# Performance work log

Hardware: AMD Instinct MI355X
Metric: run time of the kernel (lower is better)

## Reference

```python
import jax, jax.numpy as jnp
import numpy as np
import math

B, L, D, H, NL, V, C = 32, 512, 512, 8, 4, 32000, 2
DK = D // H
DFF = 4 * D
EPS = 1e-5


def _pos_encoding(max_len, d):
    pos = np.arange(max_len)[:, None].astype(np.float32)
    div = np.exp(np.arange(0, d, 2).astype(np.float32) * (-math.log(10000.0) / d))
    pe = np.zeros((max_len, d), np.float32)
    pe[:, 0::2] = np.sin(pos * div)
    pe[:, 1::2] = np.cos(pos * div)
    return jnp.asarray(pe)


def setup_inputs() -> dict:
    key = jax.random.key(0)
    keys = iter(jax.random.split(key, 64))
    s = 0.02
    def nrm(shape):
        return jax.random.normal(next(keys), shape, jnp.float32) * s
    emb = nrm((V, D)).at[0].set(0.0)  # padding_idx=0 row zeroed
    return {
        "x": jax.random.randint(next(keys), (B, L), 0, V),
        "mask": jnp.zeros((B, L), bool),
        "emb": emb,
        "pe": _pos_encoding(L, D),
        "Wq": nrm((NL, D, D)), "bq": jnp.zeros((NL, D)),
        "Wk": nrm((NL, D, D)), "bk": jnp.zeros((NL, D)),
        "Wv": nrm((NL, D, D)), "bv": jnp.zeros((NL, D)),
        "Wo": nrm((NL, D, D)), "bo": jnp.zeros((NL, D)),
        "ln1_g": jnp.ones((NL, D)), "ln1_b": jnp.zeros((NL, D)),
        "ln2_g": jnp.ones((NL, D)), "ln2_b": jnp.zeros((NL, D)),
        "ffW1": nrm((NL, D, DFF)), "ffb1": jnp.zeros((NL, DFF)),
        "ffW2": nrm((NL, DFF, D)), "ffb2": jnp.zeros((NL, D)),
        "lnf_g": jnp.ones((D,)), "lnf_b": jnp.zeros((D,)),
        "cW1": nrm((D, D)), "cb1": jnp.zeros((D,)),
        "cW2": nrm((D, C)), "cb2": jnp.zeros((C,)),
    }


def _layernorm(x, g, b):
    mu = jnp.mean(x, axis=-1, keepdims=True)
    var = jnp.mean((x - mu) ** 2, axis=-1, keepdims=True)
    return (x - mu) / jnp.sqrt(var + EPS) * g + b


def reference(x, mask, emb, pe, Wq, bq, Wk, bk, Wv, bv, Wo, bo,
              ln1_g, ln1_b, ln2_g, ln2_b, ffW1, ffb1, ffW2, ffb2,
              lnf_g, lnf_b, cW1, cb1, cW2, cb2):
    Bx, Lx = x.shape
    h = emb[x] * math.sqrt(D) + pe[None, :Lx, :]  # [B,L,D]
    key_mask = mask[:, None, None, :]  # [B,1,1,L]
    for i in range(NL):
        # --- multi-head attention (pre-norm1) ---
        hn = _layernorm(h, ln1_g[i], ln1_b[i])
        q = (hn @ Wq[i] + bq[i]).reshape(Bx, Lx, H, DK)
        k = (hn @ Wk[i] + bk[i]).reshape(Bx, Lx, H, DK)
        v = (hn @ Wv[i] + bv[i]).reshape(Bx, Lx, H, DK)
        scores = jnp.einsum('bqhd,bkhd->bhqk', q, k) / math.sqrt(DK)
        scores = jnp.where(key_mask, -jnp.inf, scores)
        attn = jax.nn.softmax(scores, axis=-1)
        ctx = jnp.einsum('bhqk,bkhd->bqhd', attn, v).reshape(Bx, Lx, D)
        h = h + ctx @ Wo[i] + bo[i]
        # --- feed-forward (pre-norm2), exact (erf) GELU like torch default ---
        hn2 = _layernorm(h, ln2_g[i], ln2_b[i])
        ff = jax.nn.gelu(hn2 @ ffW1[i] + ffb1[i], approximate=False) @ ffW2[i] + ffb2[i]
        h = h + ff
    h = _layernorm(h, lnf_g, lnf_b)
    pooled = jnp.mean(h, axis=1)  # [B,D]
    logits = jax.nn.gelu(pooled @ cW1 + cb1, approximate=False) @ cW2 + cb2
    return logits
```

## Files before the change

kernel.cpp:

```cpp
#include <hip/hip_runtime.h>
#include <hip/hip_bf16.h>

typedef __bf16 bf16_t;
typedef __bf16 bf16x8 __attribute__((ext_vector_type(8)));
typedef float  f32x4  __attribute__((ext_vector_type(4)));

#define NTOK 16384
#define DMODEL 512
#define SEQL 512
#define NLAY 4

typedef const __attribute__((address_space(1))) void* gas_t;
typedef __attribute__((address_space(3))) void* las_t;
__device__ __forceinline__ void gl16(const void* g, void* s){
  __builtin_amdgcn_global_load_lds((gas_t)g, (las_t)s, 16, 0, 0);
}

__device__ __forceinline__ f32x4 mfma16(bf16x8 a, bf16x8 b, f32x4 c){
  return __builtin_amdgcn_mfma_f32_16x16x32_bf16(a, b, c, 0, 0, 0);
}
__device__ __forceinline__ float geluf(float x){
  return 0.5f * x * (1.0f + erff(x * 0.70710678118654752f));
}
__device__ __forceinline__ float loadf(const void* p, long i, bool f32){
  return f32 ? ((const float*)p)[i] : (float)((const bf16_t*)p)[i];
}

__global__ void sniff_kernel(const unsigned int* __restrict__ emb_u, int* __restrict__ flag){
  if (threadIdx.x == 0){
    unsigned int u = emb_u[300] | emb_u[350] | emb_u[400] | emb_u[450];
    *flag = (u == 0u) ? 1 : 0;
  }
}

__global__ void transpose_kernel(const void* __restrict__ in, bf16_t* __restrict__ out,
                                 int R, int C, const int* __restrict__ flag){
  const bool f32 = (*flag != 0);
  __shared__ bf16_t tile[32][33];
  const long zo = (long)blockIdx.z * R * C;
  const int c0 = blockIdx.x * 32, r0 = blockIdx.y * 32;
  const int tx = threadIdx.x, ty = threadIdx.y;
  for (int i = 0; i < 4; i++){
    long idx = zo + (long)(r0 + ty + i*8) * C + (c0 + tx);
    tile[ty + i*8][tx] = (bf16_t)loadf(in, idx, f32);
  }
  __syncthreads();
  for (int i = 0; i < 4; i++){
    out[zo + (long)(c0 + ty + i*8) * R + (r0 + tx)] = tile[tx][ty + i*8];
  }
}

__global__ void transpose_qkv_kernel(const void* __restrict__ Wq, const void* __restrict__ Wk,
                                     const void* __restrict__ Wv, bf16_t* __restrict__ out,
                                     const int* __restrict__ flag){
  const bool f32 = (*flag != 0);
  __shared__ bf16_t tile[32][33];
  const int z = blockIdx.z, lz = z / 3, s = z % 3;
  const void* in = (s == 0) ? Wq : (s == 1) ? Wk : Wv;
  const long zi = (long)lz * 262144;
  const int c0 = blockIdx.x * 32, r0 = blockIdx.y * 32;
  const int tx = threadIdx.x, ty = threadIdx.y;
  for (int i = 0; i < 4; i++){
    long idx = zi + (long)(r0 + ty + i*8) * 512 + (c0 + tx);
    tile[ty + i*8][tx] = (bf16_t)loadf(in, idx, f32);
  }
  __syncthreads();
  for (int i = 0; i < 4; i++){
    out[(long)lz * 786432 + (long)(s*512 + c0 + ty + i*8) * 512 + (r0 + tx)] = tile[tx][ty + i*8];
  }
}

__global__ void biasprep_kernel(const void* bq, const void* bk, const void* bv,
                                const void* bo, const void* fb1, const void* fb2,
                                float* bqkvF, float* boF, float* fb1F, float* fb2F,
                                const int* __restrict__ flag){
  const bool f32 = (*flag != 0);
  const int z = blockIdx.y;
  const int idx = blockIdx.x * 256 + threadIdx.x;
  if (idx < 1536){
    const void* src = (idx < 512) ? bq : (idx < 1024) ? bk : bv;
    bqkvF[z*1536 + idx] = loadf(src, (long)z*512 + (idx & 511), f32);
  } else if (idx < 2048){
    boF[z*512 + idx - 1536] = loadf(bo, (long)z*512 + idx - 1536, f32);
  } else if (idx < 4096){
    fb1F[z*2048 + idx - 2048] = loadf(fb1, (long)z*2048 + idx - 2048, f32);
  } else {
    fb2F[z*512 + idx - 4096] = loadf(fb2, (long)z*512 + idx - 4096, f32);
  }
}

__global__ void embed_kernel(const int* __restrict__ x, const void* __restrict__ emb,
                             const void* __restrict__ pe, float* __restrict__ h,
                             const int* __restrict__ flag){
  const bool f32 = (*flag != 0);
  const int n = blockIdx.x;
  const int tok = x[n];
  const int l = n & (SEQL - 1);
  for (int d = threadIdx.x; d < DMODEL; d += 256){
    h[(long)n*DMODEL + d] = loadf(emb, (long)tok*DMODEL + d, f32) * 22.62741699796952f
                          + loadf(pe, (long)l*DMODEL + d, f32);
  }
}

__global__ void ln_kernel(const float* __restrict__ in, const void* __restrict__ g,
                          const void* __restrict__ b, long gboff, bf16_t* __restrict__ out,
                          const int* __restrict__ flag){
  const bool f32 = (*flag != 0);
  const int row = blockIdx.x, t = threadIdx.x;
  const float* r = in + (long)row * DMODEL;
  float v0 = r[t], v1 = r[t + 256];
  __shared__ float sb[4];
  float s = v0 + v1;
  #pragma unroll
  for (int o = 32; o > 0; o >>= 1) s += __shfl_down(s, o);
  if ((t & 63) == 0) sb[t >> 6] = s;
  __syncthreads();
  float mu = (sb[0] + sb[1] + sb[2] + sb[3]) * (1.f / DMODEL);
  __syncthreads();
  float d0 = v0 - mu, d1 = v1 - mu;
  s = d0*d0 + d1*d1;
  #pragma unroll
  for (int o = 32; o > 0; o >>= 1) s += __shfl_down(s, o);
  if ((t & 63) == 0) sb[t >> 6] = s;
  __syncthreads();
  float var = (sb[0] + sb[1] + sb[2] + sb[3]) * (1.f / DMODEL);
  float rstd = rsqrtf(var + 1e-5f);
  out[(long)row*DMODEL + t]       = (bf16_t)(d0*rstd*loadf(g, gboff + t, f32)       + loadf(b, gboff + t, f32));
  out[(long)row*DMODEL + t + 256] = (bf16_t)(d1*rstd*loadf(g, gboff + t + 256, f32) + loadf(b, gboff + t + 256, f32));
}

template<int MODE>
__global__ __launch_bounds__(256) void gemm_kernel(
    const bf16_t* __restrict__ A, const bf16_t* __restrict__ Bt,
    const float* __restrict__ bias,
    bf16_t* __restrict__ outB, float* __restrict__ outF, int K){
  __shared__ __align__(16) bf16_t S[4][8192];
  const int t = threadIdx.x;
  const int n0 = blockIdx.y * 128, m0 = blockIdx.x * 128;
  const int M = gridDim.x * 128;
  const int l = t & 63, w = t >> 6;
  const int lm = l & 15, g = l >> 4;
  const int wr = (w >> 1) * 64, wc = (w & 1) * 64;
  const f32x4 z4 = {0.f, 0.f, 0.f, 0.f};
  f32x4 acc[4][4];
  #pragma unroll
  for (int i = 0; i < 4; i++)
    #pragma unroll
    for (int j = 0; j < 4; j++) acc[i][j] = z4;
  const int offA0 = w*2048 + l*16;
  const int offA1 = offA0 + 1024;
  const bf16_t* gA0 = A  + (long)(n0 + (offA0 >> 6))*K + ((offA0 & 63) >> 1);
  const bf16_t* gA1 = A  + (long)(n0 + (offA1 >> 6))*K + ((offA1 & 63) >> 1);
  const bf16_t* gB0 = Bt + (long)(m0 + (offA0 >> 6))*K + ((offA0 & 63) >> 1);
  const bf16_t* gB1 = Bt + (long)(m0 + (offA1 >> 6))*K + ((offA1 & 63) >> 1);
  const int NT = K >> 5;
  #pragma unroll
  for (int pt = 0; pt < 3; ++pt){
    bf16_t* sb = &S[pt][0];
    const int ko = pt * 32;
    gl16(gA0 + ko, sb + w*1024);
    gl16(gA1 + ko, sb + w*1024 + 512);
    gl16(gB0 + ko, sb + 4096 + w*1024);
    gl16(gB1 + ko, sb + 4096 + w*1024 + 512);
  }
  for (int tt = 0; tt < NT; ++tt){
    const int tc = (tt + 3 < NT) ? (tt + 3) : (NT - 1);
    bf16_t* sb = &S[(tt + 3) & 3][0];
    const int ko = tc * 32;
    gl16(gA0 + ko, sb + w*1024);
    gl16(gA1 + ko, sb + w*1024 + 512);
    gl16(gB0 + ko, sb + 4096 + w*1024);
    gl16(gB1 + ko, sb + 4096 + w*1024 + 512);
    asm volatile("s_waitcnt vmcnt(12)" ::: "memory");
    __builtin_amdgcn_s_barrier();
    __builtin_amdgcn_sched_barrier(0);
    const bf16_t* As = &S[tt & 3][0];
    const bf16_t* Bs = As + 4096;
    bf16x8 af[4], bfr[4];
    #pragma unroll
    for (int i = 0; i < 4; i++) af[i]  = *(const bf16x8*)&As[(wr + i*16 + lm)*32 + g*8];
    #pragma unroll
    for (int j = 0; j < 4; j++) bfr[j] = *(const bf16x8*)&Bs[(wc + j*16 + lm)*32 + g*8];
    __builtin_amdgcn_s_setprio(1);
    #pragma unroll
    for (int i = 0; i < 4; i++)
      #pragma unroll
      for (int j = 0; j < 4; j++)
        acc[i][j] = mfma16(af[i], bfr[j], acc[i][j]);
    __builtin_amdgcn_s_setprio(0);
    __builtin_amdgcn_s_barrier();
    __builtin_amdgcn_sched_barrier(0);
  }
  asm volatile("s_waitcnt vmcnt(0)" ::: "memory");
  __syncthreads();
  if (MODE == 1){
    #pragma unroll
    for (int j = 0; j < 4; j++){
      const int m = m0 + wc + j*16 + lm;
      const float bv = bias[m];
      #pragma unroll
      for (int i = 0; i < 4; i++){
        const int nb = n0 + wr + i*16 + g*4;
        #pragma unroll
        for (int r = 0; r < 4; r++) outF[(long)(nb + r)*M + m] += acc[i][j][r] + bv;
      }
    }
  } else {
    bf16_t* Cs = &S[0][0] + w*1152;
    #pragma unroll
    for (int i = 0; i < 4; i++){
      #pragma unroll
      for (int j = 0; j < 4; j++){
        const float bv = bias[m0 + wc + j*16 + lm];
        #pragma unroll
        for (int r = 0; r < 4; r++){
          float v = acc[i][j][r] + bv;
          if (MODE == 2) v = geluf(v);
          Cs[(g*4 + r)*72 + j*16 + lm] = (bf16_t)v;
        }
      }
      const int row16 = l >> 2, ch = l & 3;
      #pragma unroll
      for (int cc = 0; cc < 2; cc++){
        const int chunk = cc*4 + ch;
        bf16x8 vv = *(const bf16x8*)&Cs[row16*72 + chunk*8];
        *(bf16x8*)&outB[(long)(n0 + wr + i*16 + row16)*M + m0 + wc + chunk*8] = vv;
      }
    }
  }
}

__global__ __launch_bounds__(64) void attn_kernel(
    const bf16_t* __restrict__ QKV, bf16_t* __restrict__ Op){
  const int l = threadIdx.x;
  const int lm = l & 15, g = l >> 4;
  const int qc = blockIdx.x;
  const int hh = blockIdx.y;
  const int bb = blockIdx.z;
  const long base = (long)bb * SEQL;
  const int hc = hh * 64;
  const int QS = 1536;
  const int q0 = qc * 64;
  bf16x8 qf[4][2];
  #pragma unroll
  for (int i = 0; i < 4; i++){
    const bf16_t* qrow = QKV + (base + q0 + i*16 + lm)*QS + hc + g*8;
    qf[i][0] = *(const bf16x8*)(qrow);
    qf[i][1] = *(const bf16x8*)(qrow + 32);
  }
  const f32x4 z4 = {0.f, 0.f, 0.f, 0.f};
  f32x4 oa[4][4];
  #pragma unroll
  for (int i = 0; i < 4; i++)
    #pragma unroll
    for (int dt = 0; dt < 4; dt++) oa[i][dt] = z4;
  float m_run[4], l_run[4];
  #pragma unroll
  for (int i = 0; i < 4; i++){ m_run[i] = -1e30f; l_run[i] = 0.f; }

  for (int kt = 0; kt < SEQL/32; ++kt){
    const int kcb = kt * 32;
    const bf16_t* kr0 = QKV + (base + kcb + lm)*QS + 512 + hc + g*8;
    const bf16_t* kr1 = kr0 + 16*QS;
    bf16x8 kf00 = *(const bf16x8*)(kr0);
    bf16x8 kf01 = *(const bf16x8*)(kr0 + 32);
    bf16x8 kf10 = *(const bf16x8*)(kr1);
    bf16x8 kf11 = *(const bf16x8*)(kr1 + 32);
    bf16x8 pa[4];
    #pragma unroll
    for (int i = 0; i < 4; i++){
      f32x4 s0 = z4, s1 = z4;
      __builtin_amdgcn_s_setprio(1);
      s0 = mfma16(kf00, qf[i][0], s0);
      s0 = mfma16(kf01, qf[i][1], s0);
      s1 = mfma16(kf10, qf[i][0], s1);
      s1 = mfma16(kf11, qf[i][1], s1);
      __builtin_amdgcn_s_setprio(0);
      float p[8]; float tmax = -1e30f;
      #pragma unroll
      for (int r = 0; r < 4; r++){ p[r] = s0[r]*0.125f; p[4+r] = s1[r]*0.125f; }
      #pragma unroll
      for (int j2 = 0; j2 < 8; j2++) tmax = fmaxf(tmax, p[j2]);
      tmax = fmaxf(tmax, __shfl_xor(tmax, 16));
      tmax = fmaxf(tmax, __shfl_xor(tmax, 32));
      const float mn = fmaxf(m_run[i], tmax);
      float ts = 0.f;
      #pragma unroll
      for (int j2 = 0; j2 < 8; j2++){ p[j2] = __expf(p[j2] - mn); ts += p[j2]; }
      ts += __shfl_xor(ts, 16);
      ts += __shfl_xor(ts, 32);
      const float alpha = __expf(m_run[i] - mn);
      l_run[i] = l_run[i] * alpha + ts;
      m_run[i] = mn;
      f32x4 alv;
      #pragma unroll
      for (int r = 0; r < 4; r++) alv[r] = __shfl(alpha, g*4 + r);
      #pragma unroll
      for (int dt = 0; dt < 4; dt++) oa[i][dt] *= alv;
      #pragma unroll
      for (int j2 = 0; j2 < 8; j2++) pa[i][j2] = (bf16_t)p[j2];
    }
    bf16x8 vf[4];
    #pragma unroll
    for (int j2 = 0; j2 < 8; j2++){
      const int pk = (j2 < 4) ? (g*4 + j2) : (16 + g*4 + (j2 - 4));
      const bf16_t* vr = QKV + (base + kcb + pk)*QS + 1024 + hc + lm;
      #pragma unroll
      for (int dt = 0; dt < 4; dt++) vf[dt][j2] = vr[dt*16];
    }
    __builtin_amdgcn_s_setprio(1);
    #pragma unroll
    for (int i = 0; i < 4; i++)
      #pragma unroll
      for (int dt = 0; dt < 4; dt++) oa[i][dt] = mfma16(pa[i], vf[dt], oa[i][dt]);
    __builtin_amdgcn_s_setprio(0);
  }
  #pragma unroll
  for (int i = 0; i < 4; i++){
    const float invl = 1.f / l_run[i];
    f32x4 inv;
    #pragma unroll
    for (int r = 0; r < 4; r++) inv[r] = __shfl(invl, g*4 + r);
    #pragma unroll
    for (int dt = 0; dt < 4; dt++)
      #pragma unroll
      for (int r = 0; r < 4; r++)
        Op[(base + q0 + i*16 + g*4 + r)*DMODEL + hc + dt*16 + lm] = (bf16_t)(oa[i][dt][r] * inv[r]);
  }
}

__global__ void pool_kernel(const bf16_t* __restrict__ hn, float* __restrict__ pooled){
  const int b = blockIdx.x, d = threadIdx.x;
  float a = 0.f;
  for (int s = 0; s < SEQL; s++) a += (float)hn[((long)b*SEQL + s)*DMODEL + d];
  pooled[b*DMODEL + d] = a * (1.f / SEQL);
}

__global__ void cls1_kernel(const float* __restrict__ pooled, const void* __restrict__ w1,
                            const void* __restrict__ b1, float* __restrict__ t1,
                            const int* __restrict__ flag){
  const bool f32 = (*flag != 0);
  const int b = blockIdx.x, m = threadIdx.x;
  const float* p = pooled + b * DMODEL;
  float a = 0.f;
  for (int d = 0; d < DMODEL; d++) a += p[d] * loadf(w1, (long)d*DMODEL + m, f32);
  t1[b*DMODEL + m] = geluf(a + loadf(b1, m, f32));
}

__global__ void cls2_kernel(const float* __restrict__ t1, const void* __restrict__ w2,
                            const void* __restrict__ b2, void* __restrict__ outp,
                            const int* __restrict__ flag){
  const bool f32 = (*flag != 0);
  const int i = threadIdx.x;
  if (i >= 64) return;
  const int b = i >> 1, c = i & 1;
  float a = 0.f;
  for (int m = 0; m < DMODEL; m++) a += t1[b*DMODEL + m] * loadf(w2, (long)m*2 + c, f32);
  a += loadf(b2, c, f32);
  if (f32) ((float*)outp)[i] = a;
  else     ((bf16_t*)outp)[i] = (bf16_t)a;
}

extern "C" void kernel_launch(void* const* d_in, const int* in_sizes, int n_in,
                              void* d_out, int out_size, void* d_ws, size_t ws_size,
                              hipStream_t stream){
  const int* x    = (const int*)d_in[0];
  const void* emb = d_in[2];
  const void* pe  = d_in[3];
  const void* Wq = d_in[4];  const void* bq = d_in[5];
  const void* Wk = d_in[6];  const void* bk = d_in[7];
  const void* Wv = d_in[8];  const void* bv = d_in[9];
  const void* Wo = d_in[10]; const void* bo = d_in[11];
  const void* ln1g = d_in[12]; const void* ln1b = d_in[13];
  const void* ln2g = d_in[14]; const void* ln2b = d_in[15];
  const void* fW1 = d_in[16]; const void* fb1 = d_in[17];
  const void* fW2 = d_in[18]; const void* fb2 = d_in[19];
  const void* lnfg = d_in[20]; const void* lnfb = d_in[21];
  const void* cW1 = d_in[22]; const void* cb1 = d_in[23];
  const void* cW2 = d_in[24]; const void* cb2 = d_in[25];

  char* ws = (char*)d_ws;
  float*  h     = (float*) (ws + 0);
  bf16_t* hn    = (bf16_t*)(ws + 33554432);
  bf16_t* qkv   = (bf16_t*)(ws + 50331648);
  bf16_t* ctx   = (bf16_t*)(ws + 100663296);
  bf16_t* ff1   = (bf16_t*)(ws + 50331648);
  bf16_t* WqkvT = (bf16_t*)(ws + 117440512);
  bf16_t* WoT   = (bf16_t*)(ws + 123731968);
  bf16_t* W1T   = (bf16_t*)(ws + 125829120);
  bf16_t* W2T   = (bf16_t*)(ws + 134217728);
  float*  bqkvF = (float*) (ws + 142606336);
  float*  boF   = (float*) (ws + 142630912);
  float*  fb1F  = (float*) (ws + 142639104);
  float*  fb2F  = (float*) (ws + 142671872);
  float*  pooled= (float*) (ws + 142680064);
  float*  t1    = (float*) (ws + 142745600);
  int*    flag  = (int*)   (ws + 142811136);

  sniff_kernel<<<1, 64, 0, stream>>>((const unsigned int*)emb, flag);

  dim3 tb(32, 8);
  transpose_qkv_kernel<<<dim3(16,16,12), tb, 0, stream>>>(Wq, Wk, Wv, WqkvT, flag);
  transpose_kernel<<<dim3(16,16,4), tb, 0, stream>>>(Wo,  WoT, 512, 512,  flag);
  transpose_kernel<<<dim3(64,16,4), tb, 0, stream>>>(fW1, W1T, 512, 2048, flag);
  transpose_kernel<<<dim3(16,64,4), tb, 0, stream>>>(fW2, W2T, 2048, 512, flag);
  biasprep_kernel<<<dim3(18,4), 256, 0, stream>>>(bq, bk, bv, bo, fb1, fb2,
                                                  bqkvF, boF, fb1F, fb2F, flag);

  embed_kernel<<<NTOK, 256, 0, stream>>>(x, emb, pe, h, flag);

  for (int i = 0; i < NLAY; ++i){
    ln_kernel<<<NTOK, 256, 0, stream>>>(h, ln1g, ln1b, (long)i*512, hn, flag);
    gemm_kernel<0><<<dim3(12,128), 256, 0, stream>>>(hn,  WqkvT + (long)i*786432, bqkvF + (long)i*1536, qkv, nullptr, 512);
    attn_kernel<<<dim3(8,8,32), 64, 0, stream>>>(qkv, ctx);
    gemm_kernel<1><<<dim3(4,128),  256, 0, stream>>>(ctx, WoT + (long)i*262144,  boF  + (long)i*512,  nullptr, h, 512);
    ln_kernel<<<NTOK, 256, 0, stream>>>(h, ln2g, ln2b, (long)i*512, hn, flag);
    gemm_kernel<2><<<dim3(16,128), 256, 0, stream>>>(hn,  W1T + (long)i*1048576, fb1F + (long)i*2048, ff1, nullptr, 512);
    gemm_kernel<1><<<dim3(4,128),  256, 0, stream>>>(ff1, W2T + (long)i*1048576, fb2F + (long)i*512,  nullptr, h, 2048);
  }

  ln_kernel<<<NTOK, 256, 0, stream>>>(h, lnfg, lnfb, 0, hn, flag);
  pool_kernel<<<32, 512, 0, stream>>>(hn, pooled);
  cls1_kernel<<<32, 512, 0, stream>>>(pooled, cW1, cb1, t1, flag);
  cls2_kernel<<<1, 64, 0, stream>>>(t1, cW2, cb2, d_out, flag);
}
```

Measured before the change: 1.395 ms.

## Enlarge GEMM tiles to 256-row blocks with 512 threads and XCD-aware swizzle

Rewrites the GEMM kernel to use 256xBM output tiles computed by 8 waves (512 threads) instead of 128x128 tiles with 4 waves, and launches a 1D grid remapped so neighbouring tiles land on the same XCD. The aim is more operand reuse per LDS load and better L2 locality. In exchange, the 4-deep global-to-LDS pipeline becomes double buffering, which may expose more memory latency. Fewer workgroups are launched for the narrow output-projection GEMMs, which may also leave compute units underused.

```diff
diff --git a/kernel.cpp b/kernel.cpp
--- a/kernel.cpp
+++ b/kernel.cpp
@@ -129,61 +129,65 @@
   out[(long)row*DMODEL + t + 256] = (bf16_t)(d1*rstd*loadf(g, gboff + t + 256, f32) + loadf(b, gboff + t + 256, f32));
 }
 
-template<int MODE>
-__global__ __launch_bounds__(256) void gemm_kernel(
+template<int MODE, int BM>
+__global__ __launch_bounds__(512) void gemm_kernel(
     const bf16_t* __restrict__ A, const bf16_t* __restrict__ Bt,
     const float* __restrict__ bias,
-    bf16_t* __restrict__ outB, float* __restrict__ outF, int K){
-  __shared__ __align__(16) bf16_t S[4][8192];
+    bf16_t* __restrict__ outB, float* __restrict__ outF, int K, int gx){
+  constexpr int ASLOT = 8192;
+  constexpr int BSLOT = BM * 32;
+  constexpr int SLOT  = ASLOT + BSLOT;
+  constexpr int NWR   = (BM == 256) ? 8 : 4;
+  __shared__ __align__(16) bf16_t S[2 * SLOT];
   const int t = threadIdx.x;
-  const int n0 = blockIdx.y * 128, m0 = blockIdx.x * 128;
-  const int M = gridDim.x * 128;
+  const int nwg = gridDim.x;
+  const int cpx = nwg >> 3;
+  const int flat = blockIdx.x;
+  const int swz = (flat & 7) * cpx + (flat >> 3);
+  const int m0 = (swz % gx) * BM, n0 = (swz / gx) * 256;
+  const int M = gx * BM;
   const int l = t & 63, w = t >> 6;
   const int lm = l & 15, g = l >> 4;
-  const int wr = (w >> 1) * 64, wc = (w & 1) * 64;
+  const int wr = (BM == 256) ? (w >> 2) * 128 : (w >> 1) * 64;
+  const int wc = (BM == 256) ? (w & 3) * 64  : (w & 1) * 64;
   const f32x4 z4 = {0.f, 0.f, 0.f, 0.f};
-  f32x4 acc[4][4];
-  #pragma unroll
-  for (int i = 0; i < 4; i++)
+  f32x4 acc[NWR][4];
+  #pragma unroll
+  for (int i = 0; i < NWR; i++)
     #pragma unroll
     for (int j = 0; j < 4; j++) acc[i][j] = z4;
-  const int offA0 = w*2048 + l*16;
-  const int offA1 = offA0 + 1024;
-  const bf16_t* gA0 = A  + (long)(n0 + (offA0 >> 6))*K + ((offA0 & 63) >> 1);
-  const bf16_t* gA1 = A  + (long)(n0 + (offA1 >> 6))*K + ((offA1 & 63) >> 1);
-  const bf16_t* gB0 = Bt + (long)(m0 + (offA0 >> 6))*K + ((offA0 & 63) >> 1);
-  const bf16_t* gB1 = Bt + (long)(m0 + (offA1 >> 6))*K + ((offA1 & 63) >> 1);
+  const int offA = t * 16;
+  const int ra = offA >> 6, ca = (offA & 63) >> 1;
+  const bf16_t* gA0 = A  + (long)(n0 + ra)       * K + ca;
+  const bf16_t* gA1 = A  + (long)(n0 + ra + 128) * K + ca;
+  const bf16_t* gB0 = Bt + (long)(m0 + ra)       * K + ca;
+  const bf16_t* gB1 = (BM == 256) ? (Bt + (long)(m0 + ra + 128) * K + ca) : gB0;
   const int NT = K >> 5;
-  #pragma unroll
-  for (int pt = 0; pt < 3; ++pt){
-    bf16_t* sb = &S[pt][0];
-    const int ko = pt * 32;
-    gl16(gA0 + ko, sb + w*1024);
-    gl16(gA1 + ko, sb + w*1024 + 512);
-    gl16(gB0 + ko, sb + 4096 + w*1024);
-    gl16(gB1 + ko, sb + 4096 + w*1024 + 512);
-  }
+  auto STAGE = [&](int slot, int ko){
+    bf16_t* sb = &S[slot * SLOT];
+    gl16(gA0 + ko, sb + w*512);
+    gl16(gA1 + ko, sb + 4096 + w*512);
+    gl16(gB0 + ko, sb + ASLOT + w*512);
+    if constexpr (BM == 256) gl16(gB1 + ko, sb + ASLOT + 4096 + w*512);
+  };
+  STAGE(0, 0);
   for (int tt = 0; tt < NT; ++tt){
-    const int tc = (tt + 3 < NT) ? (tt + 3) : (NT - 1);
-    bf16_t* sb = &S[(tt + 3) & 3][0];
-    const int ko = tc * 32;
-    gl16(gA0 + ko, sb + w*1024);
-    gl16(gA1 + ko, sb + w*1024 + 512);
-    gl16(gB0 + ko, sb + 4096 + w*1024);
-    gl16(gB1 + ko, sb + 4096 + w*1024 + 512);
-    asm volatile("s_waitcnt vmcnt(12)" ::: "memory");
+    const int tc = (tt + 1 < NT) ? (tt + 1) : (NT - 1);
+    STAGE((tt + 1) & 1, tc * 32);
+    if constexpr (BM == 256) asm volatile("s_waitcnt vmcnt(4)" ::: "memory");
+    else                     asm volatile("s_waitcnt vmcnt(3)" ::: "memory");
     __builtin_amdgcn_s_barrier();
     __builtin_amdgcn_sched_barrier(0);
-    const bf16_t* As = &S[tt & 3][0];
-    const bf16_t* Bs = As + 4096;
-    bf16x8 af[4], bfr[4];
-    #pragma unroll
-    for (int i = 0; i < 4; i++) af[i]  = *(const bf16x8*)&As[(wr + i*16 + lm)*32 + g*8];
-    #pragma unroll
-    for (int j = 0; j < 4; j++) bfr[j] = *(const bf16x8*)&Bs[(wc + j*16 + lm)*32 + g*8];
+    const bf16_t* As = &S[(tt & 1) * SLOT];
+    const bf16_t* Bs = As + ASLOT;
+    bf16x8 af[NWR], bfr[4];
+    #pragma unroll
+    for (int i = 0; i < NWR; i++) af[i]  = *(const bf16x8*)&As[(wr + i*16 + lm)*32 + g*8];
+    #pragma unroll
+    for (int j = 0; j < 4; j++)   bfr[j] = *(const bf16x8*)&Bs[(wc + j*16 + lm)*32 + g*8];
     __builtin_amdgcn_s_setprio(1);
     #pragma unroll
-    for (int i = 0; i < 4; i++)
+    for (int i = 0; i < NWR; i++)
       #pragma unroll
       for (int j = 0; j < 4; j++)
         acc[i][j] = mfma16(af[i], bfr[j], acc[i][j]);
@@ -199,16 +203,16 @@
       const int m = m0 + wc + j*16 + lm;
       const float bv = bias[m];
       #pragma unroll
-      for (int i = 0; i < 4; i++){
+      for (int i = 0; i < NWR; i++){
         const int nb = n0 + wr + i*16 + g*4;
         #pragma unroll
         for (int r = 0; r < 4; r++) outF[(long)(nb + r)*M + m] += acc[i][j][r] + bv;
       }
     }
   } else {
-    bf16_t* Cs = &S[0][0] + w*1152;
-    #pragma unroll
-    for (int i = 0; i < 4; i++){
+    bf16_t* Cs = &S[0] + w*1152;
+    #pragma unroll
+    for (int i = 0; i < NWR; i++){
       #pragma unroll
       for (int j = 0; j < 4; j++){
         const float bv = bias[m0 + wc + j*16 + lm];
@@ -411,12 +415,12 @@
 
   for (int i = 0; i < NLAY; ++i){
     ln_kernel<<<NTOK, 256, 0, stream>>>(h, ln1g, ln1b, (long)i*512, hn, flag);
-    gemm_kernel<0><<<dim3(12,128), 256, 0, stream>>>(hn,  WqkvT + (long)i*786432, bqkvF + (long)i*1536, qkv, nullptr, 512);
+    gemm_kernel<0,256><<<384, 512, 0, stream>>>(hn,  WqkvT + (long)i*786432, bqkvF + (long)i*1536, qkv, nullptr, 512, 6);
     attn_kernel<<<dim3(8,8,32), 64, 0, stream>>>(qkv, ctx);
-    gemm_kernel<1><<<dim3(4,128),  256, 0, stream>>>(ctx, WoT + (long)i*262144,  boF  + (long)i*512,  nullptr, h, 512);
+    gemm_kernel<1,128><<<256, 512, 0, stream>>>(ctx, WoT + (long)i*262144,  boF  + (long)i*512,  nullptr, h, 512, 4);
     ln_kernel<<<NTOK, 256, 0, stream>>>(h, ln2g, ln2b, (long)i*512, hn, flag);
-    gemm_kernel<2><<<dim3(16,128), 256, 0, stream>>>(hn,  W1T + (long)i*1048576, fb1F + (long)i*2048, ff1, nullptr, 512);
-    gemm_kernel<1><<<dim3(4,128),  256, 0, stream>>>(ff1, W2T + (long)i*1048576, fb2F + (long)i*512,  nullptr, h, 2048);
+    gemm_kernel<2,256><<<512, 512, 0, stream>>>(hn,  W1T + (long)i*1048576, fb1F + (long)i*2048, ff1, nullptr, 512, 8);
+    gemm_kernel<1,128><<<256, 512, 0, stream>>>(ff1, W2T + (long)i*1048576, fb2F + (long)i*512,  nullptr, h, 2048, 4);
   }
 
   ln_kernel<<<NTOK, 256, 0, stream>>>(h, lnfg, lnfb, 0, hn, flag);
```

New measurement: 1.355 ms. 1.03x faster.
